# Optimization experiments

Measured on AMD Instinct MI355X. Metric: run time of the kernel, lower is better.

## Reference

```python
import jax, jax.numpy as jnp
import numpy as np

DIM = 512
HEADS = 8
DH = 64
INNER = HEADS * DH  # 512
GRID = 32
FH, FW = GRID, GRID // 2 + 1


def _group_norm1(x, g, b, eps=1e-5):
    # GroupNorm(1, C) on NHWC: normalize over (H, W, C) per sample, per-channel affine
    mu = jnp.mean(x, axis=(1, 2, 3), keepdims=True)
    var = jnp.var(x, axis=(1, 2, 3), keepdims=True)
    return (x - mu) * jax.lax.rsqrt(var + eps) * g + b


def setup_inputs() -> dict:
    key = jax.random.key(0)
    ks = jax.random.split(key, 12)
    B, N, C = 8, GRID * GRID + 1, DIM
    s = 0.02
    return {
        "x": jax.random.normal(ks[0], (B, N, C), jnp.float32),
        "Wq": jax.random.normal(ks[1], (C, INNER), jnp.float32) * s,
        "Wk": jax.random.normal(ks[2], (C, INNER), jnp.float32) * s,
        "Wv": jax.random.normal(ks[3], (C, INNER), jnp.float32) * s,
        "dw_w": jax.random.normal(ks[4], (3, 3, 1, C), jnp.float32) * s,   # depthwise, HWIO
        "pw_w": jax.random.normal(ks[5], (C, INNER), jnp.float32) * s,     # 1x1 conv
        "ln_g": jnp.ones((INNER,), jnp.float32),
        "ln_b": jnp.zeros((INNER,), jnp.float32),
        "fr_wr": jnp.ones((FH, FW, C), jnp.float32),    # learnable FFT filter (real)
        "fr_wi": jnp.zeros((FH, FW, C), jnp.float32),   # learnable FFT filter (imag)
        "fr_pw": jax.random.normal(ks[6], (C, INNER), jnp.float32) * s,
        "fr_g": jnp.ones((INNER,), jnp.float32),
        "fr_b": jnp.zeros((INNER,), jnp.float32),
        "g_W1": jax.random.normal(ks[7], (3 * INNER, 3 * INNER // 4), jnp.float32) * s,
        "g_b1": jnp.zeros((3 * INNER // 4,), jnp.float32),
        "g_W2": jax.random.normal(ks[8], (3 * INNER // 4, 3), jnp.float32) * s,
        "g_b2": jnp.zeros((3,), jnp.float32),
        "Wp": jax.random.normal(ks[9], (INNER, DIM), jnp.float32) * s,
        "bp": jnp.zeros((DIM,), jnp.float32),
        "h_feat": GRID,
        "w_feat": GRID,
    }


def reference(x, Wq, Wk, Wv, dw_w, pw_w, ln_g, ln_b, fr_wr, fr_wi, fr_pw, fr_g, fr_b,
              g_W1, g_b1, g_W2, g_b2, Wp, bp, h_feat, w_feat):
    B, N, C = x.shape
    scale = DH ** -0.5
    has_cls = (N == h_feat * w_feat + 1)
    spatial = x[:, 1:] if has_cls else x

    # Branch 1: global self-attention (manual softmax attention)
    q = (x @ Wq).reshape(B, N, HEADS, DH)
    k = (x @ Wk).reshape(B, N, HEADS, DH)
    v = (x @ Wv).reshape(B, N, HEADS, DH)
    attn = jax.nn.softmax(jnp.einsum('bihd,bjhd->bhij', q, k) * scale, axis=-1)
    glob = jnp.einsum('bhij,bjhd->bihd', attn, v).reshape(B, N, INNER)

    # Branch 2: local depthwise conv -> pointwise conv -> GroupNorm(1)
    sp = spatial.reshape(B, h_feat, w_feat, C)  # NHWC
    dw = jax.lax.conv_general_dilated(sp, dw_w, (1, 1), 'SAME',
                                      dimension_numbers=('NHWC', 'HWIO', 'NHWC'),
                                      feature_group_count=C)
    loc = _group_norm1(jnp.einsum('bhwc,co->bhwo', dw, pw_w), ln_g, ln_b)
    loc = loc.reshape(B, h_feat * w_feat, INNER)
    if has_cls:
        loc = jnp.concatenate([loc.mean(axis=1, keepdims=True), loc], axis=1)

    # Branch 3: frequency enhancement (rfft2 -> learnable complex filter -> irfft2)
    xf = jnp.fft.rfft2(sp, axes=(1, 2), norm='ortho')               # (B, FH, FW, C)
    xf = xf * jax.lax.complex(fr_wr, fr_wi)[None]
    xe = jnp.fft.irfft2(xf, s=(h_feat, w_feat), axes=(1, 2), norm='ortho')
    fr = jax.nn.gelu(_group_norm1(jnp.einsum('bhwc,co->bhwo', xe, fr_pw), fr_g, fr_b),
                     approximate=False)
    fr = fr.reshape(B, h_feat * w_feat, INNER)
    if has_cls:
        fr = jnp.concatenate([fr.mean(axis=1, keepdims=True), fr], axis=1)

    # Gate MLP + softmax fusion
    cat = jnp.concatenate([glob, loc, fr], axis=-1)                  # (B, N, 3*INNER)
    gw = jax.nn.softmax(jax.nn.gelu(cat @ g_W1 + g_b1, approximate=False) @ g_W2 + g_b2,
                        axis=-1)                                     # (B, N, 3)
    fused = gw[..., 0:1] * glob + gw[..., 1:2] * loc + gw[..., 2:3] * fr
    return fused @ Wp + bp
```

## Files before the change

kernel.cpp:

```cpp
#include <hip/hip_runtime.h>
#include <math.h>

#define BB 8
#define NT 1025
#define CD 512
#define NH 8
#define DHD 64
#define HW 1024
#define FWD 17
#define MTOK 8200
#define MPAD 8320
#define QKS 1536

typedef __attribute__((ext_vector_type(8))) short short8;
typedef __attribute__((ext_vector_type(4))) float f32x4;
typedef __attribute__((ext_vector_type(16))) float f32x16;
typedef __attribute__((ext_vector_type(4))) unsigned u32x4;

__device__ __forceinline__ float gelu_exact(float x){
  return 0.5f * x * (1.0f + erff(x * 0.70710678118654752f));
}

__device__ __forceinline__ short f2bf(float f){
  unsigned u = __float_as_uint(f);
  unsigned r = (u + 0x7FFFu + ((u >> 16) & 1u)) >> 16;
  return (short)r;
}

__device__ __forceinline__ float bf2f(short s){
  unsigned u = ((unsigned)(unsigned short)s) << 16;
  return __uint_as_float(u);
}

__device__ __forceinline__ unsigned cvt_pk_bf16(float lo, float hi){
  unsigned r;
  asm volatile("v_cvt_pk_bf16_f32 %0, %1, %2" : "=v"(r) : "v"(lo), "v"(hi));
  return r;
}

__device__ __forceinline__ int xcd_logical(int phys, int n){
  int xcd = phys & 7, slot = phys >> 3;
  int q = n >> 3, r = n & 7;
  return xcd*q + (xcd < r ? xcd : r) + slot;
}

__global__ __launch_bounds__(256) void prep_all(
    const float* __restrict__ Wq, const float* __restrict__ Wk, const float* __restrict__ Wv,
    const float* __restrict__ pw, const float* __restrict__ frpw,
    const float* __restrict__ gW1, const float* __restrict__ Wp,
    short* __restrict__ wqkvt, short* __restrict__ pwt, short* __restrict__ frpwt,
    short* __restrict__ gw1t, short* __restrict__ wpt,
    const float* __restrict__ x, short* __restrict__ xb, float* __restrict__ stats)
{
  const int t = blockIdx.x;
  if (t >= 4192){
    int i0 = (t - 4192)*1024 + threadIdx.x;
    #pragma unroll
    for (int j = 0; j < 4; j++){
      int i = i0 + j*256;
      if (i < 8256) stats[i] = 0.f;
    }
    return;
  }
  if (t >= 2112){
    size_t i = ((size_t)(t - 2112)*256 + threadIdx.x) * 8;
    if (i >= (size_t)MPAD*CD) return;
    size_t row = i >> 9;
    short8 o;
    if (row < MTOK){
      #pragma unroll
      for (int j = 0; j < 8; j++) o[j] = f2bf(x[i+j]);
    } else {
      #pragma unroll
      for (int j = 0; j < 8; j++) o[j] = 0;
    }
    *(short8*)(xb + i) = o;
    return;
  }
  const float* W; short* Wt; int K, N, idx; float scale = 1.0f;
  if      (t < 256) { W = Wq;   Wt = wqkvt;            K=512;  N=512; idx=t;       scale=0.125f; }
  else if (t < 512) { W = Wk;   Wt = wqkvt+512*512;    K=512;  N=512; idx=t-256; }
  else if (t < 768) { W = Wv;   Wt = wqkvt+1024*512;   K=512;  N=512; idx=t-512; }
  else if (t < 1024){ W = pw;   Wt = pwt;              K=512;  N=512; idx=t-768; }
  else if (t < 1280){ W = frpw; Wt = frpwt;            K=512;  N=512; idx=t-1024; }
  else if (t < 1856){ W = gW1;  Wt = gw1t;             K=1536; N=384; idx=t-1280; }
  else              { W = Wp;   Wt = wpt;              K=512;  N=512; idx=t-1856; }
  const int ntn = N >> 5;
  const int n0 = (idx % ntn) << 5, k0 = (idx / ntn) << 5;
  __shared__ float tl[32][33];
  const int tx = threadIdx.x & 31, ty = threadIdx.x >> 5;
  #pragma unroll
  for (int i = 0; i < 32; i += 8)
    tl[ty+i][tx] = W[(size_t)(k0+ty+i)*N + n0+tx];
  __syncthreads();
  #pragma unroll
  for (int i = 0; i < 32; i += 8)
    Wt[(size_t)(n0+ty+i)*K + k0+tx] = f2bf(tl[tx][ty+i] * scale);
}

#define GEMM_DECL                                                          \
  __shared__ short As[128*64];                                             \
  __shared__ short Bs[64*64];                                              \
  const int tid = threadIdx.x;                                             \
  const int lane = tid & 63, wv = tid >> 6;                                \
  const int lc = lane & 15, lg = lane >> 4;                                \
  f32x4 acc[2][4];                                                         \
  _Pragma("unroll")                                                        \
  for (int rt=0;rt<2;rt++)                                                 \
    _Pragma("unroll")                                                      \
    for (int ct=0;ct<4;ct++) acc[rt][ct] = (f32x4){0.f,0.f,0.f,0.f};

#define GEMM_STAGE(Aptr, Ka, k0a, Bptr, Kb, k0b)                           \
  __syncthreads();                                                         \
  _Pragma("unroll")                                                        \
  for (int p = 0; p < 4; p++){                                             \
    int c = tid + p*256;                                                   \
    int r = c >> 3, s = c & 7;                                             \
    short8 v = *(const short8*)((Aptr) + (size_t)(row0 + r)*(Ka) + (k0a) + s*8); \
    *(short8*)&As[r*64 + ((s ^ (r & 7))*8)] = v;                           \
  }                                                                        \
  _Pragma("unroll")                                                        \
  for (int p = 0; p < 2; p++){                                             \
    int c = tid + p*256;                                                   \
    int r = c >> 3, s = c & 7;                                             \
    short8 v = *(const short8*)((Bptr) + (size_t)(col0 + r)*(Kb) + (k0b) + s*8); \
    *(short8*)&Bs[r*64 + ((s ^ (r & 7))*8)] = v;                           \
  }                                                                        \
  __syncthreads();

#define GEMM_COMPUTE                                                       \
  _Pragma("unroll")                                                        \
  for (int ks = 0; ks < 2; ks++){                                          \
    short8 af[2], bfr[4];                                                  \
    _Pragma("unroll")                                                      \
    for (int rt = 0; rt < 2; rt++){                                        \
      int r = wv*32 + rt*16 + lc;                                          \
      af[rt] = *(const short8*)&As[r*64 + (((ks*4+lg) ^ (r & 7))*8)];      \
    }                                                                      \
    _Pragma("unroll")                                                      \
    for (int ct = 0; ct < 4; ct++){                                        \
      int r = ct*16 + lc;                                                  \
      bfr[ct] = *(const short8*)&Bs[r*64 + (((ks*4+lg) ^ (r & 7))*8)];     \
    }                                                                      \
    _Pragma("unroll")                                                      \
    for (int rt = 0; rt < 2; rt++)                                         \
      _Pragma("unroll")                                                    \
      for (int ct = 0; ct < 4; ct++)                                       \
        acc[rt][ct] = __builtin_amdgcn_mfma_f32_16x16x32_bf16(af[rt], bfr[ct], acc[rt][ct], 0,0,0); \
  }

__global__ __launch_bounds__(256) void gemm_mega(
    const short* __restrict__ xb, const short* __restrict__ wqkvt, short* __restrict__ qkvb,
    const short* __restrict__ aL, const short* __restrict__ bL, short* __restrict__ cL,
    float* __restrict__ totL,
    const short* __restrict__ aF, const short* __restrict__ bF, short* __restrict__ cF,
    float* __restrict__ totF)
{
  const int l = xcd_logical(blockIdx.x, 1292);
  const short *A, *Bt; short* Cm; float* tot = nullptr;
  int N, row0, col0;
  if (l < 780){
    A = xb; Bt = wqkvt; Cm = qkvb; N = 1536;
    row0 = (l / 12) * 128; col0 = (l % 12) * 128;
  } else if (l < 1036){
    int l2 = l - 780;
    A = aL; Bt = bL; Cm = cL; tot = totL; N = 512;
    row0 = (l2 >> 2) * 128; col0 = (l2 & 3) * 128;
  } else {
    int l2 = l - 1036;
    A = aF; Bt = bF; Cm = cF; tot = totF; N = 512;
    row0 = (l2 >> 2) * 128; col0 = (l2 & 3) * 128;
  }
  const int K = 512;

  __shared__ short As[128*64];
  __shared__ short Bs[128*64];
  const int tid = threadIdx.x;
  const int lane = tid & 63, wv = tid >> 6;
  const int lc = lane & 15, lg = lane >> 4;
  f32x4 acc[2][8];
  #pragma unroll
  for (int rt=0;rt<2;rt++)
    #pragma unroll
    for (int ct=0;ct<8;ct++) acc[rt][ct] = (f32x4){0.f,0.f,0.f,0.f};

  for (int k0 = 0; k0 < K; k0 += 64){
    __syncthreads();
    #pragma unroll
    for (int p = 0; p < 4; p++){
      int c = tid + p*256;
      int r = c >> 3, s = c & 7;
      short8 v = *(const short8*)(A + (size_t)(row0 + r)*K + k0 + s*8);
      *(short8*)&As[r*64 + ((s ^ (r & 7))*8)] = v;
    }
    #pragma unroll
    for (int p = 0; p < 4; p++){
      int c = tid + p*256;
      int r = c >> 3, s = c & 7;
      short8 v = *(const short8*)(Bt + (size_t)(col0 + r)*K + k0 + s*8);
      *(short8*)&Bs[r*64 + ((s ^ (r & 7))*8)] = v;
    }
    __syncthreads();
    #pragma unroll
    for (int ks = 0; ks < 2; ks++){
      short8 af[2], bfr[8];
      #pragma unroll
      for (int rt = 0; rt < 2; rt++){
        int r = wv*32 + rt*16 + lc;
        af[rt] = *(const short8*)&As[r*64 + (((ks*4+lg) ^ (r & 7))*8)];
      }
      #pragma unroll
      for (int ct = 0; ct < 8; ct++){
        int r = ct*16 + lc;
        bfr[ct] = *(const short8*)&Bs[r*64 + (((ks*4+lg) ^ (r & 7))*8)];
      }
      #pragma unroll
      for (int rt = 0; rt < 2; rt++)
        #pragma unroll
        for (int ct = 0; ct < 8; ct++)
          acc[rt][ct] = __builtin_amdgcn_mfma_f32_16x16x32_bf16(af[rt], bfr[ct], acc[rt][ct], 0,0,0);
    }
  }

  float s1 = 0.f, s2 = 0.f;
  #pragma unroll
  for (int rt = 0; rt < 2; rt++)
    #pragma unroll
    for (int e = 0; e < 4; e++){
      int gr = row0 + wv*32 + rt*16 + lg*4 + e;
      #pragma unroll
      for (int ct = 0; ct < 8; ct++){
        int gc = col0 + ct*16 + lc;
        float v = acc[rt][ct][e];
        Cm[(size_t)gr*N + gc] = f2bf(v);
        s1 += v; s2 += v*v;
      }
    }
  if (tot){
    #pragma unroll
    for (int o = 32; o > 0; o >>= 1){ s1 += __shfl_xor(s1, o); s2 += __shfl_xor(s2, o); }
    if (lane == 0){
      atomicAdd(&tot[(row0>>10)*2],   s1);
      atomicAdd(&tot[(row0>>10)*2+1], s2);
    }
  }
}

__global__ __launch_bounds__(256) void gemm_final(
    const short* __restrict__ A, const short* __restrict__ Bt,
    const float* __restrict__ bias, float* __restrict__ Cm, int M)
{
  const int N = 512, K = 512;
  const int l = xcd_logical(blockIdx.x, gridDim.x);
  const int row0 = (l >> 3) * 128, col0 = (l & 7) * 64;
  GEMM_DECL;
  for (int k0 = 0; k0 < K; k0 += 64){
    GEMM_STAGE(A, K, k0, Bt, K, k0);
    GEMM_COMPUTE;
  }
  #pragma unroll
  for (int rt = 0; rt < 2; rt++)
    #pragma unroll
    for (int e = 0; e < 4; e++){
      int gr = row0 + wv*32 + rt*16 + lg*4 + e;
      if (gr >= M) continue;
      #pragma unroll
      for (int ct = 0; ct < 4; ct++){
        int gc = col0 + ct*16 + lc;
        Cm[(size_t)gr*N + gc] = acc[rt][ct][e] + bias[gc];
      }
    }
}

__global__ __launch_bounds__(256) void gemm_gate(
    const short* __restrict__ A0, const short* __restrict__ A1, const short* __restrict__ A2,
    const short* __restrict__ Bt, const float* __restrict__ bias, short* __restrict__ Cm,
    int M)
{
  const int N = 384, K = 1536;
  const int l = xcd_logical(blockIdx.x, gridDim.x);
  const int row0 = (l / 6) * 128, col0 = (l % 6) * 64;
  GEMM_DECL;
  for (int kt = 0; kt < 24; kt++){
    int k0 = kt * 64;
    const short* Asrc = (k0 < 512) ? A0 : (k0 < 1024 ? A1 : A2);
    const int kb = k0 & 511;
    GEMM_STAGE(Asrc, 512, kb, Bt, K, k0);
    GEMM_COMPUTE;
  }
  #pragma unroll
  for (int rt = 0; rt < 2; rt++)
    #pragma unroll
    for (int e = 0; e < 4; e++){
      int gr = row0 + wv*32 + rt*16 + lg*4 + e;
      if (gr >= M) continue;
      #pragma unroll
      for (int ct = 0; ct < 4; ct++){
        int gc = col0 + ct*16 + lc;
        float v = acc[rt][ct][e] + bias[gc];
        Cm[(size_t)gr*N + gc] = f2bf(gelu_exact(v));
      }
    }
}

__global__ __launch_bounds__(256) void attn_gn(
    const short* __restrict__ qkv, short* __restrict__ glob,
    const short* __restrict__ mmL, const short* __restrict__ mmF,
    const float* __restrict__ totL, const float* __restrict__ totF,
    const float* __restrict__ gL, const float* __restrict__ bL,
    const float* __restrict__ gF, const float* __restrict__ bF,
    short* __restrict__ loc, short* __restrict__ fr,
    float* __restrict__ colsumL, float* __restrict__ colsumF)
{
  __shared__ short Kl[2][64*64];
  __shared__ short Vl[2][64*64];

  if (blockIdx.x >= 576){
    const int bi2 = blockIdx.x - 576;
    const int br = bi2 >> 9;
    const int rem = bi2 & 511;
    const int b = rem >> 6;
    const int sub = rem & 63;
    const int p0 = (sub >> 1) << 5;
    const int c = (sub & 1)*256 + threadIdx.x;
    const short* mm = br ? mmF : mmL;
    const float* tot = br ? totF : totL;
    short* out = br ? fr : loc;
    float* colsum = br ? colsumF : colsumL;
    const float inv = 1.0f / ((float)HW * CD);
    const float mu = tot[b*2] * inv;
    const float rstd = rsqrtf(tot[b*2+1]*inv - mu*mu + 1e-5f);
    const float gc = (br ? gF : gL)[c], bc = (br ? bF : bL)[c];
    float s = 0.0f;
    for (int r = 0; r < 32; r++){
      int p = p0 + r;
      float v = bf2f(mm[((size_t)b*HW + p)*CD + c]);
      v = (v - mu) * rstd * gc + bc;
      if (br) v = gelu_exact(v);
      out[((size_t)(b*NT + 1 + p))*CD + c] = f2bf(v);
      s += v;
    }
    atomicAdd(&colsum[b*CD + c], s);
    return;
  }

  const int bi = blockIdx.x;
  const int xcd = bi & 7;
  const int jj = bi >> 3;
  const int gq = jj / 9;
  const int qt = jj - gq*9;
  const int g  = xcd + 8*gq;
  const int h  = g & 7, b = g >> 3;

  const int tid = threadIdx.x;
  const int lane = tid & 63, wq = tid >> 6;
  const int q32 = lane & 31;
  const int hi  = lane >> 5;
  const int bN = b * NT;
  const int q0w = qt*128 + wq*32;

  short8 qf[4];
  {
    int qr = q0w + q32; if (qr > 1024) qr = 1024;
    const short* qp = qkv + (size_t)(bN + qr)*QKS + h*DHD + hi*8;
    qf[0] = *(const short8*)(qp);
    qf[1] = *(const short8*)(qp + 16);
    qf[2] = *(const short8*)(qp + 32);
    qf[3] = *(const short8*)(qp + 48);
  }

  f32x16 oA = {0.f,0.f,0.f,0.f,0.f,0.f,0.f,0.f,0.f,0.f,0.f,0.f,0.f,0.f,0.f,0.f};
  f32x16 oB = oA;
  float rs = 0.f;

  const int kc0 = tid;
  const int kc1 = tid + 256;
  const int vkey = tid & 63, vdg = tid >> 6;
  const short* kgbase = qkv + (size_t)bN*QKS + 512 + h*DHD;
  const short* vgbase = qkv + (size_t)bN*QKS + 1024 + h*DHD;

  short8 gk0, gk1, gv0, gv1;
  auto loadT = [&](int kt2){
    gk0 = *(const short8*)(kgbase + (size_t)(kt2*64 + (kc0>>3))*QKS + (kc0&7)*8);
    gk1 = *(const short8*)(kgbase + (size_t)(kt2*64 + (kc1>>3))*QKS + (kc1&7)*8);
    gv0 = *(const short8*)(vgbase + (size_t)(kt2*64 + vkey)*QKS + vdg*16);
    gv1 = *(const short8*)(vgbase + (size_t)(kt2*64 + vkey)*QKS + vdg*16 + 8);
  };
  auto writeT = [&](int buf){
    { int r = kc0>>3, sl = kc0&7;
      *(short8*)&Kl[buf][r*64 + (((sl) ^ (r&7))*8)] = gk0; }
    { int r = kc1>>3, sl = kc1&7;
      *(short8*)&Kl[buf][r*64 + (((sl) ^ (r&7))*8)] = gk1; }
    #pragma unroll
    for (int i2 = 0; i2 < 8; i2++){
      int d0 = vdg*16 + i2, d1 = vdg*16 + 8 + i2;
      Vl[buf][d0*64 + (((vkey>>3) ^ (d0&7))*8) + (vkey&7)] = gv0[i2];
      Vl[buf][d1*64 + (((vkey>>3) ^ (d1&7))*8) + (vkey&7)] = gv1[i2];
    }
  };

  loadT(0);
  writeT(0);
  __syncthreads();

  for (int kt = 0; kt < 17; kt++){
    const int cur = kt & 1;
    if (kt < 16) loadT(kt+1);

    #pragma unroll
    for (int ks = 0; ks < 2; ks++){
      f32x16 s = {0.f,0.f,0.f,0.f,0.f,0.f,0.f,0.f,0.f,0.f,0.f,0.f,0.f,0.f,0.f,0.f};
      const int krow = ks*32 + q32;
      const int kbase = krow*64;
      const int kx = q32 & 7;
      __builtin_amdgcn_s_setprio(1);
      #pragma unroll
      for (int kk = 0; kk < 4; kk++){
        short8 af = *(const short8*)&Kl[cur][kbase + (((2*kk+hi) ^ kx)*8)];
        s = __builtin_amdgcn_mfma_f32_32x32x16_bf16(af, qf[kk], s, 0,0,0);
      }
      __builtin_amdgcn_s_setprio(0);
      float p[16];
      if (kt == 16){
        #pragma unroll
        for (int e = 0; e < 16; e++){
          bool valid = (ks == 0) && (e == 0) && (hi == 0);
          p[e] = valid ? __expf(s[e]) : 0.f;
        }
      } else {
        #pragma unroll
        for (int e = 0; e < 16; e++) p[e] = __expf(s[e]);
      }
      #pragma unroll
      for (int e = 0; e < 16; e++) rs += p[e];
      unsigned pk[4][2];
      #pragma unroll
      for (int g2 = 0; g2 < 4; g2++){
        pk[g2][0] = cvt_pk_bf16(p[4*g2+0], p[4*g2+1]);
        pk[g2][1] = cvt_pk_bf16(p[4*g2+2], p[4*g2+3]);
      }
      #pragma unroll
      for (int kc = 0; kc < 2; kc++){
        unsigned e00 = pk[2*kc][0],   e01 = pk[2*kc][1];
        unsigned e10 = pk[2*kc+1][0], e11 = pk[2*kc+1][1];
        unsigned t00 = (unsigned)__shfl_xor((int)e00, 32);
        unsigned t01 = (unsigned)__shfl_xor((int)e01, 32);
        unsigned t10 = (unsigned)__shfl_xor((int)e10, 32);
        unsigned t11 = (unsigned)__shfl_xor((int)e11, 32);
        u32x4 pu;
        pu[0] = hi ? t10 : e00;
        pu[1] = hi ? t11 : e01;
        pu[2] = hi ? e10 : t00;
        pu[3] = hi ? e11 : t01;
        short8 pa = *(short8*)&pu;
        const int vsl = 4*ks + 2*kc + hi;
        __builtin_amdgcn_s_setprio(1);
        {
          short8 vf0 = *(const short8*)&Vl[cur][(q32)*64      + ((vsl ^ kx)*8)];
          oA = __builtin_amdgcn_mfma_f32_32x32x16_bf16(pa, vf0, oA, 0,0,0);
          short8 vf1 = *(const short8*)&Vl[cur][(32+q32)*64   + ((vsl ^ kx)*8)];
          oB = __builtin_amdgcn_mfma_f32_32x32x16_bf16(pa, vf1, oB, 0,0,0);
        }
        __builtin_amdgcn_s_setprio(0);
      }
    }

    if (kt < 16){
      writeT(cur ^ 1);
      __syncthreads();
    }
  }

  float rs_tot = rs + __shfl_xor(rs, 32);
  #pragma unroll
  for (int e = 0; e < 16; e++){
    int rowr = (e & 3) + 8*(e >> 2) + 4*hi;
    int q = q0w + rowr;
    if (q > 1024) continue;
    float inv = 1.0f / __shfl(rs_tot, rowr);
    size_t base = (size_t)(bN + q)*CD + h*DHD + q32;
    glob[base]      = f2bf(oA[e] * inv);
    glob[base + 32] = f2bf(oB[e] * inv);
  }
}

__global__ __launch_bounds__(512) void dw_fft1(
    const short* __restrict__ xb, const float* __restrict__ w, short* __restrict__ out,
    const float* __restrict__ x, float* __restrict__ Ur, float* __restrict__ Ui)
{
  __shared__ float ct[32], st[32];
  if (blockIdx.x >= 2048){
    const int bi = blockIdx.x - 2048;
    const int c = threadIdx.x;
    const int xx = bi & 31;
    const int b = bi >> 5;
    if (c < 32){ float ang = 6.283185307179586f * c / 32.0f; ct[c] = cosf(ang); st[c] = sinf(ang); }
    __syncthreads();
    float v[32];
    #pragma unroll
    for (int y = 0; y < 32; y++) v[y] = x[((size_t)(b*NT + 1 + y*32 + xx))*CD + c];
    for (int ky = 0; ky <= 16; ky++){
      float sr = 0.f, si = 0.f;
      #pragma unroll
      for (int y = 0; y < 32; y++){
        int idx = (ky*y) & 31;
        sr += v[y]*ct[idx]; si -= v[y]*st[idx];
      }
      size_t o = ((size_t)((b*17+ky)*32+xx))*CD + c;
      Ur[o] = sr; Ui[o] = si;
    }
    return;
  }
  const int c = threadIdx.x;
  const int xx = blockIdx.x & 31;
  const int yg = (blockIdx.x >> 5) & 7;
  const int b  = blockIdx.x >> 8;
  const int y0 = yg << 2;
  float acc[4] = {0.f,0.f,0.f,0.f};
  #pragma unroll
  for (int dx = -1; dx <= 1; dx++){
    int x2 = xx + dx;
    if (x2 < 0 || x2 > 31) continue;
    float col[6];
    #pragma unroll
    for (int r = 0; r < 6; r++){
      int row = y0 - 1 + r;
      col[r] = (row >= 0 && row < 32)
             ? bf2f(xb[((size_t)(b*NT + 1 + row*32 + x2))*CD + c]) : 0.f;
    }
    float w0 = w[(0*3+dx+1)*CD + c];
    float w1 = w[(1*3+dx+1)*CD + c];
    float w2 = w[(2*3+dx+1)*CD + c];
    #pragma unroll
    for (int o = 0; o < 4; o++)
      acc[o] += col[o]*w0 + col[o+1]*w1 + col[o+2]*w2;
  }
  #pragma unroll
  for (int o = 0; o < 4; o++)
    out[((size_t)(b*HW + (y0+o)*32 + xx))*CD + c] = f2bf(acc[o]);
}

__global__ __launch_bounds__(512) void colmean_fin2(
    const float* __restrict__ colsumL, const float* __restrict__ colsumF,
    short* __restrict__ loc, short* __restrict__ fr)
{
  const int c = threadIdx.x;
  const int b = blockIdx.x & 7;
  if (blockIdx.x < 8) loc[((size_t)b*NT)*CD + c] = f2bf(colsumL[b*CD + c] * (1.0f/HW));
  else                fr [((size_t)b*NT)*CD + c] = f2bf(colsumF[b*CD + c] * (1.0f/HW));
}

__global__ __launch_bounds__(256) void fft_f2(
    const float* __restrict__ Ur, const float* __restrict__ Ui,
    const float* __restrict__ wr, const float* __restrict__ wi,
    float* __restrict__ Gr, float* __restrict__ Gi)
{
  const int c = (blockIdx.x & 1)*256 + threadIdx.x;
  const int t = blockIdx.x >> 1;
  const int ky = t % 17, b = t / 17;
  __shared__ float ct[32], st[32];
  if (threadIdx.x < 32){ float ang = 6.283185307179586f * threadIdx.x / 32.0f;
    ct[threadIdx.x] = cosf(ang); st[threadIdx.x] = sinf(ang); }
  __syncthreads();
  float ar[32], ai[32];
  #pragma unroll
  for (int kx = 0; kx < 32; kx++){ ar[kx] = 0.f; ai[kx] = 0.f; }
  #pragma unroll
  for (int xx = 0; xx < 32; xx++){
    size_t o = ((size_t)((b*17+ky)*32+xx))*CD + c;
    float ur = Ur[o], ui = Ui[o];
    #pragma unroll
    for (int kx = 0; kx < 32; kx++){
      int idx = (kx*xx) & 31;
      float cc = ct[idx], ss = st[idx];
      ar[kx] += ur*cc + ui*ss;
      ai[kx] += ui*cc - ur*ss;
    }
  }
  #pragma unroll
  for (int kx = 0; kx < FWD; kx++){
    size_t fo = ((size_t)(ky*FWD+kx))*CD + c;
    float fwr = wr[fo], fwi = wi[fo];
    size_t go = ((size_t)((b*17+kx)*32+ky))*CD + c;
    Gr[go] = ar[kx]*fwr - ai[kx]*fwi;
    Gi[go] = ar[kx]*fwi + ai[kx]*fwr;
  }
  if (ky >= 1 && ky <= 15){
    const int ky2 = 32 - ky;
    #pragma unroll
    for (int kx = 0; kx < FWD; kx++){
      int m = (32 - kx) & 31;
      size_t fo = ((size_t)(ky2*FWD+kx))*CD + c;
      float fwr = wr[fo], fwi = wi[fo];
      size_t go = ((size_t)((b*17+kx)*32+ky2))*CD + c;
      Gr[go] = ar[m]*fwr + ai[m]*fwi;
      Gi[go] = ar[m]*fwi - ai[m]*fwr;
    }
  }
}

__global__ __launch_bounds__(256) void fft_f3(
    const float* __restrict__ Gr, const float* __restrict__ Gi,
    float* __restrict__ Tr, float* __restrict__ Ti)
{
  const int c = (blockIdx.x & 1)*256 + threadIdx.x;
  const int t = blockIdx.x >> 1;
  const int kx = t % 17, b = t / 17;
  __shared__ float ct[32], st[32];
  if (threadIdx.x < 32){ float ang = 6.283185307179586f * threadIdx.x / 32.0f;
    ct[threadIdx.x] = cosf(ang); st[threadIdx.x] = sinf(ang); }
  __syncthreads();
  float tr[32], ti[32];
  #pragma unroll
  for (int y = 0; y < 32; y++){ tr[y] = 0.f; ti[y] = 0.f; }
  #pragma unroll
  for (int ky = 0; ky < 32; ky++){
    size_t go = ((size_t)((b*17+kx)*32+ky))*CD + c;
    float gr = Gr[go], gi = Gi[go];
    #pragma unroll
    for (int y = 0; y < 32; y++){
      int idx = (ky*y) & 31;
      float cc = ct[idx], ss = st[idx];
      tr[y] += gr*cc - gi*ss;
      ti[y] += gr*ss + gi*cc;
    }
  }
  #pragma unroll
  for (int y = 0; y < 32; y++){
    size_t to = ((size_t)((b*32+y)*17+kx))*CD + c;
    Tr[to] = tr[y]*(1.0f/32.0f);
    Ti[to] = ti[y]*(1.0f/32.0f);
  }
}

__global__ __launch_bounds__(512) void fft_f4(
    const float* __restrict__ Tr, const float* __restrict__ Ti, short* __restrict__ xe)
{
  const int c = threadIdx.x;
  const int y = blockIdx.x & 31;
  const int b = blockIdx.x >> 5;
  __shared__ float ct[32], st[32];
  if (c < 32){ float ang = 6.283185307179586f * c / 32.0f; ct[c] = cosf(ang); st[c] = sinf(ang); }
  __syncthreads();
  float tr[FWD], ti[FWD];
  #pragma unroll
  for (int kx = 0; kx < FWD; kx++){
    size_t o = ((size_t)((b*32+y)*17+kx))*CD + c;
    tr[kx] = Tr[o]; ti[kx] = Ti[o];
  }
  for (int x2 = 0; x2 < 32; x2++){
    float acc = tr[0] + ((x2 & 1) ? -tr[16] : tr[16]);
    #pragma unroll
    for (int k2 = 1; k2 < 16; k2++){
      int idx = (k2*x2) & 31;
      acc += 2.0f*(tr[k2]*ct[idx] - ti[k2]*st[idx]);
    }
    xe[((size_t)(b*HW + y*32 + x2))*CD + c] = f2bf(acc*(1.0f/32.0f));
  }
}

__global__ __launch_bounds__(256) void gate_fuse(
    const short* __restrict__ h1, const float* __restrict__ gW2, const float* __restrict__ gb2,
    const short* __restrict__ glob, const short* __restrict__ loc, const short* __restrict__ fr,
    short* __restrict__ fused)
{
  const int token = blockIdx.x*4 + (threadIdx.x >> 6);
  const int lane = threadIdx.x & 63;
  if (token >= MTOK) return;
  float p0 = 0.f, p1 = 0.f, p2 = 0.f;
  #pragma unroll
  for (int i = 0; i < 6; i++){
    int idx = lane + i*64;
    float h = bf2f(h1[(size_t)token*384 + idx]);
    p0 += h * gW2[idx*3+0]; p1 += h * gW2[idx*3+1]; p2 += h * gW2[idx*3+2];
  }
  #pragma unroll
  for (int o = 32; o > 0; o >>= 1){
    p0 += __shfl_xor(p0, o); p1 += __shfl_xor(p1, o); p2 += __shfl_xor(p2, o);
  }
  p0 += gb2[0]; p1 += gb2[1]; p2 += gb2[2];
  float mx = fmaxf(p0, fmaxf(p1, p2));
  float e0 = __expf(p0-mx), e1 = __expf(p1-mx), e2 = __expf(p2-mx);
  float inv = 1.0f/(e0+e1+e2);
  float g0 = e0*inv, g1 = e1*inv, g2 = e2*inv;
  #pragma unroll
  for (int i = 0; i < 8; i++){
    size_t o2 = (size_t)token*CD + lane + i*64;
    fused[o2] = f2bf(g0*bf2f(glob[o2]) + g1*bf2f(loc[o2]) + g2*bf2f(fr[o2]));
  }
}

extern "C" void kernel_launch(void* const* d_in, const int* in_sizes, int n_in,
                              void* d_out, int out_size, void* d_ws, size_t ws_size,
                              hipStream_t stream)
{
  const float* x     = (const float*)d_in[0];
  const float* Wq    = (const float*)d_in[1];
  const float* Wk    = (const float*)d_in[2];
  const float* Wv    = (const float*)d_in[3];
  const float* dw_w  = (const float*)d_in[4];
  const float* pw_w  = (const float*)d_in[5];
  const float* ln_g  = (const float*)d_in[6];
  const float* ln_b  = (const float*)d_in[7];
  const float* fr_wr = (const float*)d_in[8];
  const float* fr_wi = (const float*)d_in[9];
  const float* fr_pw = (const float*)d_in[10];
  const float* fr_g  = (const float*)d_in[11];
  const float* fr_b  = (const float*)d_in[12];
  const float* g_W1  = (const float*)d_in[13];
  const float* g_b1  = (const float*)d_in[14];
  const float* g_W2  = (const float*)d_in[15];
  const float* g_b2  = (const float*)d_in[16];
  const float* Wp    = (const float*)d_in[17];
  const float* bp    = (const float*)d_in[18];

  float* ws = (float*)d_ws;
  float* scrA = ws;
  float* scrB = scrA + 8388608;
  float* stats = scrB + 4456448;
  float* totL    = stats;
  float* totF    = stats + 16;
  float* colsumL = stats + 64;
  float* colsumF = stats + 64 + 4096;

  const size_t RPAD = 8448;
  short* glob  = (short*)(stats + 16384);
  short* loc   = glob  + RPAD*CD;
  short* fr    = loc   + RPAD*CD;
  short* actbL = fr    + RPAD*CD;
  short* actbF = actbL + RPAD*CD;
  short* fused = actbL;
  short* qkvb  = actbF + RPAD*CD;
  short* xb    = qkvb + (size_t)MPAD*QKS;
  short* wqkvt = xb + (size_t)MPAD*CD;
  short* pwt   = wqkvt + 1536*512;
  short* frpwt = pwt + 512*512;
  short* gw1t  = frpwt + 512*512;
  short* wpt   = gw1t + 384*1536;
  short* mmL = (short*)scrA;
  short* mmF = mmL + (size_t)8192*CD;

  prep_all<<<4201, 256, 0, stream>>>(Wq, Wk, Wv, pw_w, fr_pw, g_W1, Wp,
                                     wqkvt, pwt, frpwt, gw1t, wpt, x, xb, stats);

  float* Ur = scrA;            float* Ui = scrA + 2228224;
  float* Gr = scrB;            float* Gi = scrB + 2228224;
  float* Tr = scrA;            float* Ti = scrA + 2228224;
  dw_fft1<<<2304, 512, 0, stream>>>(xb, dw_w, actbL, x, Ur, Ui);
  fft_f2<<<BB*17*2, 256, 0, stream>>>(Ur, Ui, fr_wr, fr_wi, Gr, Gi);
  fft_f3<<<BB*17*2, 256, 0, stream>>>(Gr, Gi, Tr, Ti);
  fft_f4<<<BB*32, 512, 0, stream>>>(Tr, Ti, actbF);

  gemm_mega<<<1292, 256, 0, stream>>>(xb, wqkvt, qkvb,
                                      actbL, pwt, mmL, totL,
                                      actbF, frpwt, mmF, totF);

  attn_gn<<<1600, 256, 0, stream>>>(qkvb, glob, mmL, mmF, totL, totF,
                                    ln_g, ln_b, fr_g, fr_b,
                                    loc, fr, colsumL, colsumF);
  colmean_fin2<<<16, 512, 0, stream>>>(colsumL, colsumF, loc, fr);

  gemm_gate<<<390, 256, 0, stream>>>(glob, loc, fr, gw1t, g_b1, (short*)scrB, MTOK);
  gate_fuse<<<2050, 256, 0, stream>>>((short*)scrB, g_W2, g_b2, glob, loc, fr, fused);
  gemm_final<<<520, 256, 0, stream>>>(fused, wpt, bp, (float*)d_out, MTOK);
}
```

Measured before the change: 266.0 us.

## Regroup kernels: co-schedule FFT stage with QKV GEMM, attention with loc/freq GEMMs, fuse gating into final GEMM

The FFT column stage now runs as extra blocks inside the QKV projection GEMM launch. Attention blocks move into the loc/freq projection GEMM launch, so independent work overlaps and kernel boundaries drop. The gate kernel now only emits the three softmax weights per token. The weighted mix of glob/loc/fr is folded into the A-tile load of the final projection GEMM, which removes the fused intermediate buffer. In exchange, the final GEMM reads three inputs per tile and recomputes the mix once per column block. The workspace layout shifts to hold the gate weights.

```diff
diff --git a/kernel.cpp b/kernel.cpp
--- a/kernel.cpp
+++ b/kernel.cpp
@@ -98,252 +98,155 @@
     Wt[(size_t)(n0+ty+i)*K + k0+tx] = f2bf(tl[tx][ty+i] * scale);
 }
 
-#define GEMM_DECL                                                          \
-  __shared__ short As[128*64];                                             \
-  __shared__ short Bs[64*64];                                              \
-  const int tid = threadIdx.x;                                             \
-  const int lane = tid & 63, wv = tid >> 6;                                \
-  const int lc = lane & 15, lg = lane >> 4;                                \
-  f32x4 acc[2][4];                                                         \
-  _Pragma("unroll")                                                        \
-  for (int rt=0;rt<2;rt++)                                                 \
-    _Pragma("unroll")                                                      \
-    for (int ct=0;ct<4;ct++) acc[rt][ct] = (f32x4){0.f,0.f,0.f,0.f};
-
-#define GEMM_STAGE(Aptr, Ka, k0a, Bptr, Kb, k0b)                           \
-  __syncthreads();                                                         \
-  _Pragma("unroll")                                                        \
-  for (int p = 0; p < 4; p++){                                             \
-    int c = tid + p*256;                                                   \
-    int r = c >> 3, s = c & 7;                                             \
-    short8 v = *(const short8*)((Aptr) + (size_t)(row0 + r)*(Ka) + (k0a) + s*8); \
-    *(short8*)&As[r*64 + ((s ^ (r & 7))*8)] = v;                           \
-  }                                                                        \
-  _Pragma("unroll")                                                        \
-  for (int p = 0; p < 2; p++){                                             \
-    int c = tid + p*256;                                                   \
-    int r = c >> 3, s = c & 7;                                             \
-    short8 v = *(const short8*)((Bptr) + (size_t)(col0 + r)*(Kb) + (k0b) + s*8); \
-    *(short8*)&Bs[r*64 + ((s ^ (r & 7))*8)] = v;                           \
-  }                                                                        \
-  __syncthreads();
-
-#define GEMM_COMPUTE                                                       \
-  _Pragma("unroll")                                                        \
-  for (int ks = 0; ks < 2; ks++){                                          \
-    short8 af[2], bfr[4];                                                  \
-    _Pragma("unroll")                                                      \
-    for (int rt = 0; rt < 2; rt++){                                        \
-      int r = wv*32 + rt*16 + lc;                                          \
-      af[rt] = *(const short8*)&As[r*64 + (((ks*4+lg) ^ (r & 7))*8)];      \
-    }                                                                      \
-    _Pragma("unroll")                                                      \
-    for (int ct = 0; ct < 4; ct++){                                        \
-      int r = ct*16 + lc;                                                  \
-      bfr[ct] = *(const short8*)&Bs[r*64 + (((ks*4+lg) ^ (r & 7))*8)];     \
-    }                                                                      \
-    _Pragma("unroll")                                                      \
-    for (int rt = 0; rt < 2; rt++)                                         \
-      _Pragma("unroll")                                                    \
-      for (int ct = 0; ct < 4; ct++)                                       \
-        acc[rt][ct] = __builtin_amdgcn_mfma_f32_16x16x32_bf16(af[rt], bfr[ct], acc[rt][ct], 0,0,0); \
-  }
-
-__global__ __launch_bounds__(256) void gemm_mega(
+#define MEGA128(Aptr, Btptr, Cptr, Nv, totptr)                              \
+{                                                                           \
+  const int K = 512;                                                        \
+  short* As = smem; short* Bs = smem + 8192;                                \
+  const int tid = threadIdx.x;                                              \
+  const int lane = tid & 63, wv = tid >> 6;                                 \
+  const int lc = lane & 15, lg = lane >> 4;                                 \
+  f32x4 acc[2][8];                                                          \
+  _Pragma("unroll")                                                         \
+  for (int rt=0;rt<2;rt++)                                                  \
+    _Pragma("unroll")                                                       \
+    for (int ct=0;ct<8;ct++) acc[rt][ct] = (f32x4){0.f,0.f,0.f,0.f};        \
+  for (int k0 = 0; k0 < K; k0 += 64){                                       \
+    __syncthreads();                                                        \
+    _Pragma("unroll")                                                       \
+    for (int p = 0; p < 4; p++){                                            \
+      int c = tid + p*256; int r = c >> 3, s = c & 7;                       \
+      short8 v = *(const short8*)((Aptr) + (size_t)(row0 + r)*K + k0 + s*8);\
+      *(short8*)&As[r*64 + ((s ^ (r & 7))*8)] = v;                          \
+    }                                                                       \
+    _Pragma("unroll")                                                       \
+    for (int p = 0; p < 4; p++){                                            \
+      int c = tid + p*256; int r = c >> 3, s = c & 7;                       \
+      short8 v = *(const short8*)((Btptr) + (size_t)(col0 + r)*K + k0 + s*8);\
+      *(short8*)&Bs[r*64 + ((s ^ (r & 7))*8)] = v;                          \
+    }                                                                       \
+    __syncthreads();                                                        \
+    _Pragma("unroll")                                                       \
+    for (int ks = 0; ks < 2; ks++){                                         \
+      short8 af[2], bfr[8];                                                 \
+      _Pragma("unroll")                                                     \
+      for (int rt = 0; rt < 2; rt++){ int r = wv*32 + rt*16 + lc;           \
+        af[rt] = *(const short8*)&As[r*64 + (((ks*4+lg) ^ (r & 7))*8)]; }   \
+      _Pragma("unroll")                                                     \
+      for (int ct = 0; ct < 8; ct++){ int r = ct*16 + lc;                   \
+        bfr[ct] = *(const short8*)&Bs[r*64 + (((ks*4+lg) ^ (r & 7))*8)]; }  \
+      _Pragma("unroll")                                                     \
+      for (int rt = 0; rt < 2; rt++)                                        \
+        _Pragma("unroll")                                                   \
+        for (int ct = 0; ct < 8; ct++)                                      \
+          acc[rt][ct] = __builtin_amdgcn_mfma_f32_16x16x32_bf16(af[rt], bfr[ct], acc[rt][ct], 0,0,0); \
+    }                                                                       \
+  }                                                                         \
+  float s1 = 0.f, s2 = 0.f;                                                 \
+  _Pragma("unroll")                                                         \
+  for (int rt = 0; rt < 2; rt++)                                            \
+    _Pragma("unroll")                                                       \
+    for (int e = 0; e < 4; e++){                                            \
+      int gr = row0 + wv*32 + rt*16 + lg*4 + e;                             \
+      _Pragma("unroll")                                                     \
+      for (int ct = 0; ct < 8; ct++){                                       \
+        int gc = col0 + ct*16 + lc;                                         \
+        float v = acc[rt][ct][e];                                           \
+        (Cptr)[(size_t)gr*(Nv) + gc] = f2bf(v);                             \
+        s1 += v; s2 += v*v;                                                 \
+      }                                                                     \
+    }                                                                       \
+  if (totptr){                                                              \
+    _Pragma("unroll")                                                       \
+    for (int o = 32; o > 0; o >>= 1){ s1 += __shfl_xor(s1, o); s2 += __shfl_xor(s2, o); } \
+    if (lane == 0){ atomicAdd(&(totptr)[(row0>>10)*2], s1);                 \
+                    atomicAdd(&(totptr)[(row0>>10)*2+1], s2); }             \
+  }                                                                         \
+}
+
+__global__ __launch_bounds__(256) void gemm_megaA(
     const short* __restrict__ xb, const short* __restrict__ wqkvt, short* __restrict__ qkvb,
+    const float* __restrict__ Ur, const float* __restrict__ Ui,
+    const float* __restrict__ wr, const float* __restrict__ wi,
+    float* __restrict__ Gr, float* __restrict__ Gi)
+{
+  __shared__ short smem[16384];
+  if (blockIdx.x >= 780){
+    float* ct = (float*)smem;
+    float* st = ct + 32;
+    const int bi = blockIdx.x - 780;
+    const int c = (bi & 1)*256 + threadIdx.x;
+    const int t = bi >> 1;
+    const int ky = t % 17, b = t / 17;
+    if (threadIdx.x < 32){ float ang = 6.283185307179586f * threadIdx.x / 32.0f;
+      ct[threadIdx.x] = cosf(ang); st[threadIdx.x] = sinf(ang); }
+    __syncthreads();
+    float ar[32], ai[32];
+    #pragma unroll
+    for (int kx = 0; kx < 32; kx++){ ar[kx] = 0.f; ai[kx] = 0.f; }
+    #pragma unroll
+    for (int xx = 0; xx < 32; xx++){
+      size_t o = ((size_t)((b*17+ky)*32+xx))*CD + c;
+      float ur = Ur[o], ui = Ui[o];
+      #pragma unroll
+      for (int kx = 0; kx < 32; kx++){
+        int idx = (kx*xx) & 31;
+        float cc = ct[idx], ss = st[idx];
+        ar[kx] += ur*cc + ui*ss;
+        ai[kx] += ui*cc - ur*ss;
+      }
+    }
+    #pragma unroll
+    for (int kx = 0; kx < FWD; kx++){
+      size_t fo = ((size_t)(ky*FWD+kx))*CD + c;
+      float fwr = wr[fo], fwi = wi[fo];
+      size_t go = ((size_t)((b*17+kx)*32+ky))*CD + c;
+      Gr[go] = ar[kx]*fwr - ai[kx]*fwi;
+      Gi[go] = ar[kx]*fwi + ai[kx]*fwr;
+    }
+    if (ky >= 1 && ky <= 15){
+      const int ky2 = 32 - ky;
+      #pragma unroll
+      for (int kx = 0; kx < FWD; kx++){
+        int m = (32 - kx) & 31;
+        size_t fo = ((size_t)(ky2*FWD+kx))*CD + c;
+        float fwr = wr[fo], fwi = wi[fo];
+        size_t go = ((size_t)((b*17+kx)*32+ky2))*CD + c;
+        Gr[go] = ar[m]*fwr + ai[m]*fwi;
+        Gi[go] = ar[m]*fwi - ai[m]*fwr;
+      }
+    }
+    return;
+  }
+  const int l = xcd_logical(blockIdx.x, 780);
+  const int row0 = (l / 12) * 128, col0 = (l % 12) * 128;
+  float* nulltot = nullptr;
+  MEGA128(xb, wqkvt, qkvb, 1536, nulltot);
+}
+
+__global__ __launch_bounds__(256) void gemm_megaB(
+    const short* __restrict__ qkv, short* __restrict__ glob,
     const short* __restrict__ aL, const short* __restrict__ bL, short* __restrict__ cL,
     float* __restrict__ totL,
     const short* __restrict__ aF, const short* __restrict__ bF, short* __restrict__ cF,
     float* __restrict__ totF)
 {
-  const int l = xcd_logical(blockIdx.x, 1292);
-  const short *A, *Bt; short* Cm; float* tot = nullptr;
-  int N, row0, col0;
-  if (l < 780){
-    A = xb; Bt = wqkvt; Cm = qkvb; N = 1536;
-    row0 = (l / 12) * 128; col0 = (l % 12) * 128;
-  } else if (l < 1036){
-    int l2 = l - 780;
-    A = aL; Bt = bL; Cm = cL; tot = totL; N = 512;
-    row0 = (l2 >> 2) * 128; col0 = (l2 & 3) * 128;
-  } else {
-    int l2 = l - 1036;
-    A = aF; Bt = bF; Cm = cF; tot = totF; N = 512;
-    row0 = (l2 >> 2) * 128; col0 = (l2 & 3) * 128;
-  }
-  const int K = 512;
-
-  __shared__ short As[128*64];
-  __shared__ short Bs[128*64];
-  const int tid = threadIdx.x;
-  const int lane = tid & 63, wv = tid >> 6;
-  const int lc = lane & 15, lg = lane >> 4;
-  f32x4 acc[2][8];
-  #pragma unroll
-  for (int rt=0;rt<2;rt++)
-    #pragma unroll
-    for (int ct=0;ct<8;ct++) acc[rt][ct] = (f32x4){0.f,0.f,0.f,0.f};
-
-  for (int k0 = 0; k0 < K; k0 += 64){
-    __syncthreads();
-    #pragma unroll
-    for (int p = 0; p < 4; p++){
-      int c = tid + p*256;
-      int r = c >> 3, s = c & 7;
-      short8 v = *(const short8*)(A + (size_t)(row0 + r)*K + k0 + s*8);
-      *(short8*)&As[r*64 + ((s ^ (r & 7))*8)] = v;
-    }
-    #pragma unroll
-    for (int p = 0; p < 4; p++){
-      int c = tid + p*256;
-      int r = c >> 3, s = c & 7;
-      short8 v = *(const short8*)(Bt + (size_t)(col0 + r)*K + k0 + s*8);
-      *(short8*)&Bs[r*64 + ((s ^ (r & 7))*8)] = v;
-    }
-    __syncthreads();
-    #pragma unroll
-    for (int ks = 0; ks < 2; ks++){
-      short8 af[2], bfr[8];
-      #pragma unroll
-      for (int rt = 0; rt < 2; rt++){
-        int r = wv*32 + rt*16 + lc;
-        af[rt] = *(const short8*)&As[r*64 + (((ks*4+lg) ^ (r & 7))*8)];
-      }
-      #pragma unroll
-      for (int ct = 0; ct < 8; ct++){
-        int r = ct*16 + lc;
-        bfr[ct] = *(const short8*)&Bs[r*64 + (((ks*4+lg) ^ (r & 7))*8)];
-      }
-      #pragma unroll
-      for (int rt = 0; rt < 2; rt++)
-        #pragma unroll
-        for (int ct = 0; ct < 8; ct++)
-          acc[rt][ct] = __builtin_amdgcn_mfma_f32_16x16x32_bf16(af[rt], bfr[ct], acc[rt][ct], 0,0,0);
-    }
-  }
-
-  float s1 = 0.f, s2 = 0.f;
-  #pragma unroll
-  for (int rt = 0; rt < 2; rt++)
-    #pragma unroll
-    for (int e = 0; e < 4; e++){
-      int gr = row0 + wv*32 + rt*16 + lg*4 + e;
-      #pragma unroll
-      for (int ct = 0; ct < 8; ct++){
-        int gc = col0 + ct*16 + lc;
-        float v = acc[rt][ct][e];
-        Cm[(size_t)gr*N + gc] = f2bf(v);
-        s1 += v; s2 += v*v;
-      }
-    }
-  if (tot){
-    #pragma unroll
-    for (int o = 32; o > 0; o >>= 1){ s1 += __shfl_xor(s1, o); s2 += __shfl_xor(s2, o); }
-    if (lane == 0){
-      atomicAdd(&tot[(row0>>10)*2],   s1);
-      atomicAdd(&tot[(row0>>10)*2+1], s2);
-    }
-  }
-}
-
-__global__ __launch_bounds__(256) void gemm_final(
-    const short* __restrict__ A, const short* __restrict__ Bt,
-    const float* __restrict__ bias, float* __restrict__ Cm, int M)
-{
-  const int N = 512, K = 512;
-  const int l = xcd_logical(blockIdx.x, gridDim.x);
-  const int row0 = (l >> 3) * 128, col0 = (l & 7) * 64;
-  GEMM_DECL;
-  for (int k0 = 0; k0 < K; k0 += 64){
-    GEMM_STAGE(A, K, k0, Bt, K, k0);
-    GEMM_COMPUTE;
-  }
-  #pragma unroll
-  for (int rt = 0; rt < 2; rt++)
-    #pragma unroll
-    for (int e = 0; e < 4; e++){
-      int gr = row0 + wv*32 + rt*16 + lg*4 + e;
-      if (gr >= M) continue;
-      #pragma unroll
-      for (int ct = 0; ct < 4; ct++){
-        int gc = col0 + ct*16 + lc;
-        Cm[(size_t)gr*N + gc] = acc[rt][ct][e] + bias[gc];
-      }
-    }
-}
-
-__global__ __launch_bounds__(256) void gemm_gate(
-    const short* __restrict__ A0, const short* __restrict__ A1, const short* __restrict__ A2,
-    const short* __restrict__ Bt, const float* __restrict__ bias, short* __restrict__ Cm,
-    int M)
-{
-  const int N = 384, K = 1536;
-  const int l = xcd_logical(blockIdx.x, gridDim.x);
-  const int row0 = (l / 6) * 128, col0 = (l % 6) * 64;
-  GEMM_DECL;
-  for (int kt = 0; kt < 24; kt++){
-    int k0 = kt * 64;
-    const short* Asrc = (k0 < 512) ? A0 : (k0 < 1024 ? A1 : A2);
-    const int kb = k0 & 511;
-    GEMM_STAGE(Asrc, 512, kb, Bt, K, k0);
-    GEMM_COMPUTE;
-  }
-  #pragma unroll
-  for (int rt = 0; rt < 2; rt++)
-    #pragma unroll
-    for (int e = 0; e < 4; e++){
-      int gr = row0 + wv*32 + rt*16 + lg*4 + e;
-      if (gr >= M) continue;
-      #pragma unroll
-      for (int ct = 0; ct < 4; ct++){
-        int gc = col0 + ct*16 + lc;
-        float v = acc[rt][ct][e] + bias[gc];
-        Cm[(size_t)gr*N + gc] = f2bf(gelu_exact(v));
-      }
-    }
-}
-
-__global__ __launch_bounds__(256) void attn_gn(
-    const short* __restrict__ qkv, short* __restrict__ glob,
-    const short* __restrict__ mmL, const short* __restrict__ mmF,
-    const float* __restrict__ totL, const float* __restrict__ totF,
-    const float* __restrict__ gL, const float* __restrict__ bL,
-    const float* __restrict__ gF, const float* __restrict__ bF,
-    short* __restrict__ loc, short* __restrict__ fr,
-    float* __restrict__ colsumL, float* __restrict__ colsumF)
-{
-  __shared__ short Kl[2][64*64];
-  __shared__ short Vl[2][64*64];
-
+  __shared__ short smem[16384];
   if (blockIdx.x >= 576){
     const int bi2 = blockIdx.x - 576;
-    const int br = bi2 >> 9;
-    const int rem = bi2 & 511;
-    const int b = rem >> 6;
-    const int sub = rem & 63;
-    const int p0 = (sub >> 1) << 5;
-    const int c = (sub & 1)*256 + threadIdx.x;
-    const short* mm = br ? mmF : mmL;
-    const float* tot = br ? totF : totL;
-    short* out = br ? fr : loc;
-    float* colsum = br ? colsumF : colsumL;
-    const float inv = 1.0f / ((float)HW * CD);
-    const float mu = tot[b*2] * inv;
-    const float rstd = rsqrtf(tot[b*2+1]*inv - mu*mu + 1e-5f);
-    const float gc = (br ? gF : gL)[c], bc = (br ? bF : bL)[c];
-    float s = 0.0f;
-    for (int r = 0; r < 32; r++){
-      int p = p0 + r;
-      float v = bf2f(mm[((size_t)b*HW + p)*CD + c]);
-      v = (v - mu) * rstd * gc + bc;
-      if (br) v = gelu_exact(v);
-      out[((size_t)(b*NT + 1 + p))*CD + c] = f2bf(v);
-      s += v;
-    }
-    atomicAdd(&colsum[b*CD + c], s);
+    const int l2 = xcd_logical(bi2, 512);
+    const int br = l2 >> 8;
+    const int t = l2 & 255;
+    const short* A  = br ? aF : aL;
+    const short* Bt = br ? bF : bL;
+    short* Cm       = br ? cF : cL;
+    float* tot      = br ? totF : totL;
+    const int row0 = (t >> 2)*128, col0 = (t & 3)*128;
+    MEGA128(A, Bt, Cm, 512, tot);
     return;
   }
 
+  short* KlB = smem;
+  short* VlB = smem + 8192;
   const int bi = blockIdx.x;
   const int xcd = bi & 7;
   const int jj = bi >> 3;
@@ -353,11 +256,11 @@
   const int h  = g & 7, b = g >> 3;
 
   const int tid = threadIdx.x;
-  const int lane = tid & 63, wq = tid >> 6;
+  const int lane = tid & 63;
   const int q32 = lane & 31;
   const int hi  = lane >> 5;
   const int bN = b * NT;
-  const int q0w = qt*128 + wq*32;
+  const int q0w = qt*128 + (tid >> 6)*32;
 
   short8 qf[4];
   {
@@ -388,14 +291,14 @@
   };
   auto writeT = [&](int buf){
     { int r = kc0>>3, sl = kc0&7;
-      *(short8*)&Kl[buf][r*64 + (((sl) ^ (r&7))*8)] = gk0; }
+      *(short8*)&KlB[buf*4096 + r*64 + ((sl ^ (r&7))*8)] = gk0; }
     { int r = kc1>>3, sl = kc1&7;
-      *(short8*)&Kl[buf][r*64 + (((sl) ^ (r&7))*8)] = gk1; }
+      *(short8*)&KlB[buf*4096 + r*64 + ((sl ^ (r&7))*8)] = gk1; }
     #pragma unroll
     for (int i2 = 0; i2 < 8; i2++){
       int d0 = vdg*16 + i2, d1 = vdg*16 + 8 + i2;
-      Vl[buf][d0*64 + (((vkey>>3) ^ (d0&7))*8) + (vkey&7)] = gv0[i2];
-      Vl[buf][d1*64 + (((vkey>>3) ^ (d1&7))*8) + (vkey&7)] = gv1[i2];
+      VlB[buf*4096 + d0*64 + (((vkey>>3) ^ (d0&7))*8) + (vkey&7)] = gv0[i2];
+      VlB[buf*4096 + d1*64 + (((vkey>>3) ^ (d1&7))*8) + (vkey&7)] = gv1[i2];
     }
   };
 
@@ -416,7 +319,7 @@
       __builtin_amdgcn_s_setprio(1);
       #pragma unroll
       for (int kk = 0; kk < 4; kk++){
-        short8 af = *(const short8*)&Kl[cur][kbase + (((2*kk+hi) ^ kx)*8)];
+        short8 af = *(const short8*)&KlB[cur*4096 + kbase + (((2*kk+hi) ^ kx)*8)];
         s = __builtin_amdgcn_mfma_f32_32x32x16_bf16(af, qf[kk], s, 0,0,0);
       }
       __builtin_amdgcn_s_setprio(0);
@@ -456,9 +359,9 @@
         const int vsl = 4*ks + 2*kc + hi;
         __builtin_amdgcn_s_setprio(1);
         {
-          short8 vf0 = *(const short8*)&Vl[cur][(q32)*64      + ((vsl ^ kx)*8)];
+          short8 vf0 = *(const short8*)&VlB[cur*4096 + (q32)*64    + ((vsl ^ kx)*8)];
           oA = __builtin_amdgcn_mfma_f32_32x32x16_bf16(pa, vf0, oA, 0,0,0);
-          short8 vf1 = *(const short8*)&Vl[cur][(32+q32)*64   + ((vsl ^ kx)*8)];
+          short8 vf1 = *(const short8*)&VlB[cur*4096 + (32+q32)*64 + ((vsl ^ kx)*8)];
           oB = __builtin_amdgcn_mfma_f32_32x32x16_bf16(pa, vf1, oB, 0,0,0);
         }
         __builtin_amdgcn_s_setprio(0);
@@ -482,6 +385,51 @@
     glob[base]      = f2bf(oA[e] * inv);
     glob[base + 32] = f2bf(oB[e] * inv);
   }
+}
+
+__global__ __launch_bounds__(256) void gn_only(
+    const short* __restrict__ mmL, const short* __restrict__ mmF,
+    const float* __restrict__ totL, const float* __restrict__ totF,
+    const float* __restrict__ gL, const float* __restrict__ bL,
+    const float* __restrict__ gF, const float* __restrict__ bF,
+    short* __restrict__ loc, short* __restrict__ fr,
+    float* __restrict__ colsumL, float* __restrict__ colsumF)
+{
+  const int bi2 = blockIdx.x;
+  const int br = bi2 >> 9;
+  const int rem = bi2 & 511;
+  const int b = rem >> 6;
+  const int sub = rem & 63;
+  const int p0 = (sub >> 1) << 5;
+  const int c = (sub & 1)*256 + threadIdx.x;
+  const short* mm = br ? mmF : mmL;
+  const float* tot = br ? totF : totL;
+  short* out = br ? fr : loc;
+  float* colsum = br ? colsumF : colsumL;
+  const float inv = 1.0f / ((float)HW * CD);
+  const float mu = tot[b*2] * inv;
+  const float rstd = rsqrtf(tot[b*2+1]*inv - mu*mu + 1e-5f);
+  const float gc = (br ? gF : gL)[c], bc = (br ? bF : bL)[c];
+  float s = 0.0f;
+  for (int r = 0; r < 32; r++){
+    int p = p0 + r;
+    float v = bf2f(mm[((size_t)b*HW + p)*CD + c]);
+    v = (v - mu) * rstd * gc + bc;
+    if (br) v = gelu_exact(v);
+    out[((size_t)(b*NT + 1 + p))*CD + c] = f2bf(v);
+    s += v;
+  }
+  atomicAdd(&colsum[b*CD + c], s);
+}
+
+__global__ __launch_bounds__(512) void colmean_fin2(
+    const float* __restrict__ colsumL, const float* __restrict__ colsumF,
+    short* __restrict__ loc, short* __restrict__ fr)
+{
+  const int c = threadIdx.x;
+  const int b = blockIdx.x & 7;
+  if (blockIdx.x < 8) loc[((size_t)b*NT)*CD + c] = f2bf(colsumL[b*CD + c] * (1.0f/HW));
+  else                fr [((size_t)b*NT)*CD + c] = f2bf(colsumF[b*CD + c] * (1.0f/HW));
 }
 
 __global__ __launch_bounds__(512) void dw_fft1(
@@ -540,65 +488,6 @@
     out[((size_t)(b*HW + (y0+o)*32 + xx))*CD + c] = f2bf(acc[o]);
 }
 
-__global__ __launch_bounds__(512) void colmean_fin2(
-    const float* __restrict__ colsumL, const float* __restrict__ colsumF,
-    short* __restrict__ loc, short* __restrict__ fr)
-{
-  const int c = threadIdx.x;
-  const int b = blockIdx.x & 7;
-  if (blockIdx.x < 8) loc[((size_t)b*NT)*CD + c] = f2bf(colsumL[b*CD + c] * (1.0f/HW));
-  else                fr [((size_t)b*NT)*CD + c] = f2bf(colsumF[b*CD + c] * (1.0f/HW));
-}
-
-__global__ __launch_bounds__(256) void fft_f2(
-    const float* __restrict__ Ur, const float* __restrict__ Ui,
-    const float* __restrict__ wr, const float* __restrict__ wi,
-    float* __restrict__ Gr, float* __restrict__ Gi)
-{
-  const int c = (blockIdx.x & 1)*256 + threadIdx.x;
-  const int t = blockIdx.x >> 1;
-  const int ky = t % 17, b = t / 17;
-  __shared__ float ct[32], st[32];
-  if (threadIdx.x < 32){ float ang = 6.283185307179586f * threadIdx.x / 32.0f;
-    ct[threadIdx.x] = cosf(ang); st[threadIdx.x] = sinf(ang); }
-  __syncthreads();
-  float ar[32], ai[32];
-  #pragma unroll
-  for (int kx = 0; kx < 32; kx++){ ar[kx] = 0.f; ai[kx] = 0.f; }
-  #pragma unroll
-  for (int xx = 0; xx < 32; xx++){
-    size_t o = ((size_t)((b*17+ky)*32+xx))*CD + c;
-    float ur = Ur[o], ui = Ui[o];
-    #pragma unroll
-    for (int kx = 0; kx < 32; kx++){
-      int idx = (kx*xx) & 31;
-      float cc = ct[idx], ss = st[idx];
-      ar[kx] += ur*cc + ui*ss;
-      ai[kx] += ui*cc - ur*ss;
-    }
-  }
-  #pragma unroll
-  for (int kx = 0; kx < FWD; kx++){
-    size_t fo = ((size_t)(ky*FWD+kx))*CD + c;
-    float fwr = wr[fo], fwi = wi[fo];
-    size_t go = ((size_t)((b*17+kx)*32+ky))*CD + c;
-    Gr[go] = ar[kx]*fwr - ai[kx]*fwi;
-    Gi[go] = ar[kx]*fwi + ai[kx]*fwr;
-  }
-  if (ky >= 1 && ky <= 15){
-    const int ky2 = 32 - ky;
-    #pragma unroll
-    for (int kx = 0; kx < FWD; kx++){
-      int m = (32 - kx) & 31;
-      size_t fo = ((size_t)(ky2*FWD+kx))*CD + c;
-      float fwr = wr[fo], fwi = wi[fo];
-      size_t go = ((size_t)((b*17+kx)*32+ky2))*CD + c;
-      Gr[go] = ar[m]*fwr + ai[m]*fwi;
-      Gi[go] = ar[m]*fwi - ai[m]*fwr;
-    }
-  }
-}
-
 __global__ __launch_bounds__(256) void fft_f3(
     const float* __restrict__ Gr, const float* __restrict__ Gi,
     float* __restrict__ Tr, float* __restrict__ Ti)
@@ -659,10 +548,83 @@
   }
 }
 
-__global__ __launch_bounds__(256) void gate_fuse(
+__global__ __launch_bounds__(256) void gemm_gate(
+    const short* __restrict__ A0, const short* __restrict__ A1, const short* __restrict__ A2,
+    const short* __restrict__ Bt, const float* __restrict__ bias, short* __restrict__ Cm,
+    int M)
+{
+  const int N = 384, K = 1536;
+  const int l = xcd_logical(blockIdx.x, gridDim.x);
+  const int row0 = (l / 6) * 128, col0 = (l % 6) * 64;
+  __shared__ short As[128*64];
+  __shared__ short Bs[64*64];
+  const int tid = threadIdx.x;
+  const int lane = tid & 63, wv = tid >> 6;
+  const int lc = lane & 15, lg = lane >> 4;
+  f32x4 acc[2][4];
+  #pragma unroll
+  for (int rt=0;rt<2;rt++)
+    #pragma unroll
+    for (int ct=0;ct<4;ct++) acc[rt][ct] = (f32x4){0.f,0.f,0.f,0.f};
+
+  for (int kt = 0; kt < 24; kt++){
+    int k0 = kt * 64;
+    const short* Asrc = (k0 < 512) ? A0 : (k0 < 1024 ? A1 : A2);
+    const int kb = k0 & 511;
+    __syncthreads();
+    #pragma unroll
+    for (int p = 0; p < 4; p++){
+      int c = tid + p*256;
+      int r = c >> 3, s = c & 7;
+      short8 v = *(const short8*)(Asrc + (size_t)(row0 + r)*512 + kb + s*8);
+      *(short8*)&As[r*64 + ((s ^ (r & 7))*8)] = v;
+    }
+    #pragma unroll
+    for (int p = 0; p < 2; p++){
+      int c = tid + p*256;
+      int r = c >> 3, s = c & 7;
+      short8 v = *(const short8*)(Bt + (size_t)(col0 + r)*K + k0 + s*8);
+      *(short8*)&Bs[r*64 + ((s ^ (r & 7))*8)] = v;
+    }
+    __syncthreads();
+    #pragma unroll
+    for (int ks = 0; ks < 2; ks++){
+      short8 af[2], bfr[4];
+      #pragma unroll
+      for (int rt = 0; rt < 2; rt++){
+        int r = wv*32 + rt*16 + lc;
+        af[rt] = *(const short8*)&As[r*64 + (((ks*4+lg) ^ (r & 7))*8)];
+      }
+      #pragma unroll
+      for (int ct = 0; ct < 4; ct++){
+        int r = ct*16 + lc;
+        bfr[ct] = *(const short8*)&Bs[r*64 + (((ks*4+lg) ^ (r & 7))*8)];
+      }
+      #pragma unroll
+      for (int rt = 0; rt < 2; rt++)
+        #pragma unroll
+        for (int ct = 0; ct < 4; ct++)
+          acc[rt][ct] = __builtin_amdgcn_mfma_f32_16x16x32_bf16(af[rt], bfr[ct], acc[rt][ct], 0,0,0);
+    }
+  }
+  #pragma unroll
+  for (int rt = 0; rt < 2; rt++)
+    #pragma unroll
+    for (int e = 0; e < 4; e++){
+      int gr = row0 + wv*32 + rt*16 + lg*4 + e;
+      if (gr >= M) continue;
+      #pragma unroll
+      for (int ct = 0; ct < 4; ct++){
+        int gc = col0 + ct*16 + lc;
+        float v = acc[rt][ct][e] + bias[gc];
+        Cm[(size_t)gr*N + gc] = f2bf(gelu_exact(v));
+      }
+    }
+}
+
+__global__ __launch_bounds__(256) void gate_gw(
     const short* __restrict__ h1, const float* __restrict__ gW2, const float* __restrict__ gb2,
-    const short* __restrict__ glob, const short* __restrict__ loc, const short* __restrict__ fr,
-    short* __restrict__ fused)
+    float* __restrict__ gw)
 {
   const int token = blockIdx.x*4 + (threadIdx.x >> 6);
   const int lane = threadIdx.x & 63;
@@ -678,16 +640,94 @@
   for (int o = 32; o > 0; o >>= 1){
     p0 += __shfl_xor(p0, o); p1 += __shfl_xor(p1, o); p2 += __shfl_xor(p2, o);
   }
-  p0 += gb2[0]; p1 += gb2[1]; p2 += gb2[2];
-  float mx = fmaxf(p0, fmaxf(p1, p2));
-  float e0 = __expf(p0-mx), e1 = __expf(p1-mx), e2 = __expf(p2-mx);
-  float inv = 1.0f/(e0+e1+e2);
-  float g0 = e0*inv, g1 = e1*inv, g2 = e2*inv;
-  #pragma unroll
-  for (int i = 0; i < 8; i++){
-    size_t o2 = (size_t)token*CD + lane + i*64;
-    fused[o2] = f2bf(g0*bf2f(glob[o2]) + g1*bf2f(loc[o2]) + g2*bf2f(fr[o2]));
-  }
+  if (lane == 0){
+    p0 += gb2[0]; p1 += gb2[1]; p2 += gb2[2];
+    float mx = fmaxf(p0, fmaxf(p1, p2));
+    float e0 = __expf(p0-mx), e1 = __expf(p1-mx), e2 = __expf(p2-mx);
+    float inv = 1.0f/(e0+e1+e2);
+    gw[token*4+0] = e0*inv;
+    gw[token*4+1] = e1*inv;
+    gw[token*4+2] = e2*inv;
+  }
+}
+
+__global__ __launch_bounds__(256) void gemm_final(
+    const short* __restrict__ glob, const short* __restrict__ loc, const short* __restrict__ fr,
+    const float* __restrict__ gw, const short* __restrict__ Bt,
+    const float* __restrict__ bias, float* __restrict__ Cm, int M)
+{
+  const int N = 512, K = 512;
+  const int l = xcd_logical(blockIdx.x, gridDim.x);
+  const int row0 = (l >> 3) * 128, col0 = (l & 7) * 64;
+  __shared__ short As[128*64];
+  __shared__ short Bs[64*64];
+  const int tid = threadIdx.x;
+  const int lane = tid & 63, wv = tid >> 6;
+  const int lc = lane & 15, lg = lane >> 4;
+  f32x4 acc[2][4];
+  #pragma unroll
+  for (int rt=0;rt<2;rt++)
+    #pragma unroll
+    for (int ct=0;ct<4;ct++) acc[rt][ct] = (f32x4){0.f,0.f,0.f,0.f};
+
+  for (int k0 = 0; k0 < K; k0 += 64){
+    __syncthreads();
+    #pragma unroll
+    for (int p = 0; p < 4; p++){
+      int c = tid + p*256;
+      int r = c >> 3, s = c & 7;
+      int gr = row0 + r;
+      float g0 = gw[gr*4+0], g1 = gw[gr*4+1], g2 = gw[gr*4+2];
+      size_t off = (size_t)gr*K + k0 + s*8;
+      short8 va = *(const short8*)(glob + off);
+      short8 vb = *(const short8*)(loc + off);
+      short8 vc = *(const short8*)(fr + off);
+      short8 o;
+      #pragma unroll
+      for (int j = 0; j < 8; j++)
+        o[j] = f2bf(g0*bf2f(va[j]) + g1*bf2f(vb[j]) + g2*bf2f(vc[j]));
+      *(short8*)&As[r*64 + ((s ^ (r & 7))*8)] = o;
+    }
+    #pragma unroll
+    for (int p = 0; p < 2; p++){
+      int c = tid + p*256;
+      int r = c >> 3, s = c & 7;
+      short8 v = *(const short8*)(Bt + (size_t)(col0 + r)*K + k0 + s*8);
+      *(short8*)&Bs[r*64 + ((s ^ (r & 7))*8)] = v;
+    }
+    __syncthreads();
+    #pragma unroll
+    for (int ks = 0; ks < 2; ks++){
+      short8 af[2], bfr[4];
+      #pragma unroll
+      for (int rt = 0; rt < 2; rt++){
+        int r = wv*32 + rt*16 + lc;
+        af[rt] = *(const short8*)&As[r*64 + (((ks*4+lg) ^ (r & 7))*8)];
+      }
+      #pragma unroll
+      for (int ct = 0; ct < 4; ct++){
+        int r = ct*16 + lc;
+        bfr[ct] = *(const short8*)&Bs[r*64 + (((ks*4+lg) ^ (r & 7))*8)];
+      }
+      #pragma unroll
+      for (int rt = 0; rt < 2; rt++)
+        #pragma unroll
+        for (int ct = 0; ct < 4; ct++)
+          acc[rt][ct] = __builtin_amdgcn_mfma_f32_16x16x32_bf16(af[rt], bfr[ct], acc[rt][ct], 0,0,0);
+    }
+  }
+  #pragma unroll
+  for (int rt = 0; rt < 2; rt++)
+    #pragma unroll
+    for (int e = 0; e < 4; e++){
+      int gr = row0 + wv*32 + rt*16 + lg*4 + e;
+      if (gr >= M) continue;
+      #pragma unroll
+      for (int ct = 0; ct < 4; ct++){
+        int gc = col0 + ct*16 + lc;
+        Cm[(size_t)gr*N + gc] = acc[rt][ct][e] + bias[gc];
+      }
+    }
 }
 
 extern "C" void kernel_launch(void* const* d_in, const int* in_sizes, int n_in,
@@ -722,14 +762,14 @@
   float* totF    = stats + 16;
   float* colsumL = stats + 64;
   float* colsumF = stats + 64 + 4096;
+  float* gw      = stats + 8448;
 
   const size_t RPAD = 8448;
-  short* glob  = (short*)(stats + 16384);
+  short* glob  = (short*)(stats + 49152);
   short* loc   = glob  + RPAD*CD;
   short* fr    = loc   + RPAD*CD;
   short* actbL = fr    + RPAD*CD;
   short* actbF = actbL + RPAD*CD;
-  short* fused = actbL;
   short* qkvb  = actbF + RPAD*CD;
   short* xb    = qkvb + (size_t)MPAD*QKS;
   short* wqkvt = xb + (size_t)MPAD*CD;
@@ -747,20 +787,21 @@
   float* Gr = scrB;            float* Gi = scrB + 2228224;
   float* Tr = scrA;            float* Ti = scrA + 2228224;
   dw_fft1<<<2304, 512, 0, stream>>>(xb, dw_w, actbL, x, Ur, Ui);
-  fft_f2<<<BB*17*2, 256, 0, stream>>>(Ur, Ui, fr_wr, fr_wi, Gr, Gi);
+
+  gemm_megaA<<<1052, 256, 0, stream>>>(xb, wqkvt, qkvb, Ur, Ui, fr_wr, fr_wi, Gr, Gi);
+
   fft_f3<<<BB*17*2, 256, 0, stream>>>(Gr, Gi, Tr, Ti);
   fft_f4<<<BB*32, 512, 0, stream>>>(Tr, Ti, actbF);
 
-  gemm_mega<<<1292, 256, 0, stream>>>(xb, wqkvt, qkvb,
-                                      actbL, pwt, mmL, totL,
-                                      actbF, frpwt, mmF, totF);
-
-  attn_gn<<<1600, 256, 0, stream>>>(qkvb, glob, mmL, mmF, totL, totF,
-                                    ln_g, ln_b, fr_g, fr_b,
+  gemm_megaB<<<1088, 256, 0, stream>>>(qkvb, glob,
+                                       actbL, pwt, mmL, totL,
+                                       actbF, frpwt, mmF, totF);
+
+  gn_only<<<1024, 256, 0, stream>>>(mmL, mmF, totL, totF, ln_g, ln_b, fr_g, fr_b,
                                     loc, fr, colsumL, colsumF);
   colmean_fin2<<<16, 512, 0, stream>>>(colsumL, colsumF, loc, fr);
 
   gemm_gate<<<390, 256, 0, stream>>>(glob, loc, fr, gw1t, g_b1, (short*)scrB, MTOK);
-  gate_fuse<<<2050, 256, 0, stream>>>((short*)scrB, g_W2, g_b2, glob, loc, fr, fused);
-  gemm_final<<<520, 256, 0, stream>>>(fused, wpt, bp, (float*)d_out, MTOK);
-}
+  gate_gw<<<2050, 256, 0, stream>>>((short*)scrB, g_W2, g_b2, gw);
+  gemm_final<<<520, 256, 0, stream>>>(glob, loc, fr, gw, wpt, bp, (float*)d_out, MTOK);
+}
```

Measured after the change: 290.5 us. 1.09x slower.
